# Performance work log

Measured on AMD Instinct MI355X. Metric: run time of the kernel, lower is better.

Reference implementation:

```python
import jax, jax.numpy as jnp
import numpy as np

B = 16384       # batch of weight blocks
IN = 64         # input_size == e_dim
DENC = 512      # dim_encoder
NRES = 2        # n_resblock (weights shared, see ResidualStack [block]*n)
NE = 2048       # n_embeddings
P = 12          # basis vectors per block
BETA = 0.25
SCALE = 1.0
SHIFT = 0.0


def setup_inputs() -> dict:
    key = jax.random.key(0)
    ks = jax.random.split(key, 6)
    s = 0.02
    return {
        "x": jax.random.normal(ks[0], (B, IN), dtype=jnp.float32),
        "enc_w1": jax.random.normal(ks[1], (IN, DENC), dtype=jnp.float32) * s,
        "enc_b1": jnp.zeros((DENC,), jnp.float32),
        "res_w": jax.random.normal(ks[2], (DENC, DENC), dtype=jnp.float32) * s,
        "res_b": jnp.zeros((DENC,), jnp.float32),
        "res_g": jnp.ones((DENC,), jnp.float32),
        "res_beta": jnp.zeros((DENC,), jnp.float32),
        "enc_w2": jax.random.normal(ks[3], (DENC, IN * P), dtype=jnp.float32) * s,
        "enc_b2": jnp.zeros((IN * P,), jnp.float32),
        "emb": jax.random.uniform(ks[4], (NE, IN), jnp.float32, -1.0 / NE, 1.0 / NE),
    }


def _layer_norm(r, g, b):
    mu = jnp.mean(r, axis=-1, keepdims=True)
    var = jnp.mean((r - mu) ** 2, axis=-1, keepdims=True)
    return (r - mu) * jax.lax.rsqrt(var + 1e-5) * g + b


def reference(x, enc_w1, enc_b1, res_w, res_b, res_g, res_beta, enc_w2, enc_b2, emb):
    sg = jax.lax.stop_gradient
    x_shift = (x - SHIFT) / SCALE

    # encoder: Linear -> (shared ResBlock) x NRES -> Linear
    h = x_shift @ enc_w1 + enc_b1                      # (B, DENC)
    for _ in range(NRES):
        h = h + jax.nn.relu(_layer_norm(h @ res_w + res_b, res_g, res_beta))
    z = h @ enc_w2 + enc_b2                            # (B, P*IN)

    z_e = z.reshape(B, P, IN)
    zf = z_e.reshape(-1, IN)                           # (B*P, IN)

    # pairwise squared distances to codebook, argmin, gather
    d = (jnp.sum(zf ** 2, axis=1, keepdims=True)
         + jnp.sum(emb ** 2, axis=1)
         - 2.0 * zf @ emb.T)                           # (B*P, NE)
    idx = jnp.argmin(d, axis=1)                        # (B*P,)
    z_q = emb[idx].reshape(B, P, IN)

    loss = (jnp.mean((sg(z_q) - z_e) ** 2)
            + BETA * jnp.mean((z_q - sg(z_e)) ** 2))

    # straight-through estimator
    z_q = z_e + sg(z_q - z_e)

    counts = jnp.zeros((NE,), jnp.float32).at[idx].add(1.0) / idx.shape[0]
    perplexity = jnp.exp(-jnp.sum(counts * jnp.log(counts + 1e-10)))

    # pinv-based reconstruction: A (B, IN, P), coeff = pinv(A) @ x_shift
    A = jnp.transpose(z_q, (0, 2, 1))                  # (B, IN, P)
    coeff = jnp.matmul(jnp.linalg.pinv(A), x_shift[..., None])  # (B, P, 1)
    x_hat = jnp.matmul(A, coeff)[..., 0]               # (B, IN)
    x_hat = SCALE * x_hat + SHIFT

    return (loss, x_hat, perplexity, idx, coeff)
```

## Files before the change

### kernel.cpp

```cpp
#include <hip/hip_runtime.h>
#include <math.h>

#define B_    16384
#define IN_   64
#define DENC_ 512
#define NE_   2048
#define P_    12
#define ROWS_ 196608
#define BETA_ 0.25

#define XHAT_OFF 1
#define PERP_OFF 1048577
#define IDXF_OFF 1048578
#define COEF_OFF 1245186

typedef __bf16 bf16x8 __attribute__((ext_vector_type(8)));
typedef float  f32x16 __attribute__((ext_vector_type(16)));

__device__ __forceinline__ void split3(float v, __bf16& h, __bf16& m, __bf16& l) {
    h = (__bf16)v;
    float r1 = v - (float)h;
    m = (__bf16)r1;
    float r2 = r1 - (float)m;
    l = (__bf16)r2;
}

__device__ __forceinline__ void gload_lds16(const void* g, void* l) {
    __builtin_amdgcn_global_load_lds((const __attribute__((address_space(1))) void*)g,
                                     (__attribute__((address_space(3))) void*)l, 16, 0, 0);
}

__global__ void k_wsplit(const float* __restrict__ W,
                         __bf16* __restrict__ Wh, __bf16* __restrict__ Wm,
                         __bf16* __restrict__ Wl, int kshift, int N, int total) {
    int idx = blockIdx.x * 256 + threadIdx.x;
    if (idx < total) {
        int n = idx >> kshift;
        int k = idx & ((1 << kshift) - 1);
        float v = W[(size_t)k * N + n];
        __bf16 h, m, l;
        split3(v, h, m, l);
        Wh[idx] = h; Wm[idx] = m; Wl[idx] = l;
    }
}

__global__ __launch_bounds__(256) void k_gemm_mfma(const float* __restrict__ A,
                                                   const __bf16* __restrict__ Bh,
                                                   const __bf16* __restrict__ Bm,
                                                   const __bf16* __restrict__ Bl,
                                                   const float* __restrict__ bias,
                                                   float* __restrict__ C,
                                                   int N, int K) {
    __shared__ __bf16 eS[2][3][64 * 64];

    const int tid = threadIdx.x;
    const int w = tid >> 6, lane = tid & 63;
    const int r0 = blockIdx.y * 128 + w * 32;
    const int n0 = blockIdx.x * 64;
    const int lrow = lane & 31;
    const int half = lane >> 5;

    const int cc0 = tid >> 3, qq = tid & 7;
    const int cc1 = cc0 + 32;
    const size_t off0 = (size_t)cc0 * K + (size_t)((qq ^ (cc0 & 7)) * 8);
    const size_t off1 = (size_t)cc1 * K + (size_t)((qq ^ (cc1 & 7)) * 8);
    const size_t nbase = (size_t)n0 * K;
    const int ld0 = w * 512;
    const int ld1 = 2048 + w * 512;

    f32x16 acc0, acc1;
#pragma unroll
    for (int i = 0; i < 16; ++i) { acc0[i] = 0.0f; acc1[i] = 0.0f; }

    {
        const size_t b = nbase;
        gload_lds16(Bh + b + off0, &eS[0][0][ld0]);
        gload_lds16(Bh + b + off1, &eS[0][0][ld1]);
        gload_lds16(Bm + b + off0, &eS[0][1][ld0]);
        gload_lds16(Bm + b + off1, &eS[0][1][ld1]);
        gload_lds16(Bl + b + off0, &eS[0][2][ld0]);
        gload_lds16(Bl + b + off1, &eS[0][2][ld1]);
    }

    const int nch = K >> 6;
    for (int ch = 0; ch < nch; ++ch) {
        const int cur = ch & 1;
        __syncthreads();

        if (ch + 1 < nch) {
            const int nxt = cur ^ 1;
            const size_t b = nbase + (size_t)(ch + 1) * 64;
            gload_lds16(Bh + b + off0, &eS[nxt][0][ld0]);
            gload_lds16(Bh + b + off1, &eS[nxt][0][ld1]);
            gload_lds16(Bm + b + off0, &eS[nxt][1][ld0]);
            gload_lds16(Bm + b + off1, &eS[nxt][1][ld1]);
            gload_lds16(Bl + b + off0, &eS[nxt][2][ld0]);
            gload_lds16(Bl + b + off1, &eS[nxt][2][ld1]);
        }

        bf16x8 ah[4], am[4], al[4];
        {
            const float* ar = A + (size_t)(r0 + lrow) * K + ch * 64 + half * 8;
#pragma unroll
            for (int kc = 0; kc < 4; ++kc) {
                float4 u0 = *(const float4*)(ar + kc * 16);
                float4 u1 = *(const float4*)(ar + kc * 16 + 4);
                float v[8] = {u0.x, u0.y, u0.z, u0.w, u1.x, u1.y, u1.z, u1.w};
#pragma unroll
                for (int j = 0; j < 8; ++j) {
                    __bf16 hh, mm, ll;
                    split3(v[j], hh, mm, ll);
                    ah[kc][j] = hh; am[kc][j] = mm; al[kc][j] = ll;
                }
            }
        }

#pragma unroll
        for (int kc = 0; kc < 4; ++kc) {
            const int q = kc * 2 + half;
            const int g = (q ^ (lrow & 7)) * 8;
            bf16x8 b0h = *(const bf16x8*)(&eS[cur][0][lrow * 64 + g]);
            bf16x8 b0m = *(const bf16x8*)(&eS[cur][1][lrow * 64 + g]);
            bf16x8 b0l = *(const bf16x8*)(&eS[cur][2][lrow * 64 + g]);
            bf16x8 b1h = *(const bf16x8*)(&eS[cur][0][(lrow + 32) * 64 + g]);
            bf16x8 b1m = *(const bf16x8*)(&eS[cur][1][(lrow + 32) * 64 + g]);
            bf16x8 b1l = *(const bf16x8*)(&eS[cur][2][(lrow + 32) * 64 + g]);

            acc0 = __builtin_amdgcn_mfma_f32_32x32x16_bf16(ah[kc], b0h, acc0, 0, 0, 0);
            acc1 = __builtin_amdgcn_mfma_f32_32x32x16_bf16(ah[kc], b1h, acc1, 0, 0, 0);
            acc0 = __builtin_amdgcn_mfma_f32_32x32x16_bf16(ah[kc], b0m, acc0, 0, 0, 0);
            acc1 = __builtin_amdgcn_mfma_f32_32x32x16_bf16(ah[kc], b1m, acc1, 0, 0, 0);
            acc0 = __builtin_amdgcn_mfma_f32_32x32x16_bf16(am[kc], b0h, acc0, 0, 0, 0);
            acc1 = __builtin_amdgcn_mfma_f32_32x32x16_bf16(am[kc], b1h, acc1, 0, 0, 0);
            acc0 = __builtin_amdgcn_mfma_f32_32x32x16_bf16(ah[kc], b0l, acc0, 0, 0, 0);
            acc1 = __builtin_amdgcn_mfma_f32_32x32x16_bf16(ah[kc], b1l, acc1, 0, 0, 0);
            acc0 = __builtin_amdgcn_mfma_f32_32x32x16_bf16(am[kc], b0m, acc0, 0, 0, 0);
            acc1 = __builtin_amdgcn_mfma_f32_32x32x16_bf16(am[kc], b1m, acc1, 0, 0, 0);
            acc0 = __builtin_amdgcn_mfma_f32_32x32x16_bf16(al[kc], b0h, acc0, 0, 0, 0);
            acc1 = __builtin_amdgcn_mfma_f32_32x32x16_bf16(al[kc], b1h, acc1, 0, 0, 0);
        }
    }

    const int col0 = n0 + lrow, col1 = col0 + 32;
    const float bv0 = bias[col0], bv1 = bias[col1];
#pragma unroll
    for (int r = 0; r < 16; ++r) {
        int row = r0 + (r & 3) + 8 * (r >> 2) + 4 * half;
        C[(size_t)row * N + col0] = acc0[r] + bv0;
        C[(size_t)row * N + col1] = acc1[r] + bv1;
    }
}

__global__ __launch_bounds__(256) void k_lnrelu(const float* __restrict__ t,
                                                float* __restrict__ h,
                                                const float* __restrict__ g,
                                                const float* __restrict__ beta) {
    const int tid = threadIdx.x;
    const int wv = tid >> 6, lane = tid & 63;
    const int row = blockIdx.x * 4 + wv;
    const float* tr = t + (size_t)row * DENC_;
    float* hr = h + (size_t)row * DENC_;

    float4 v0 = *(const float4*)(tr + lane * 4);
    float4 v1 = *(const float4*)(tr + 256 + lane * 4);

    float s = v0.x + v0.y + v0.z + v0.w + v1.x + v1.y + v1.z + v1.w;
#pragma unroll
    for (int m = 1; m < 64; m <<= 1) s += __shfl_xor(s, m);
    float mu = s / 512.0f;

    float d0x = v0.x - mu, d0y = v0.y - mu, d0z = v0.z - mu, d0w = v0.w - mu;
    float d1x = v1.x - mu, d1y = v1.y - mu, d1z = v1.z - mu, d1w = v1.w - mu;
    float vs = d0x * d0x + d0y * d0y + d0z * d0z + d0w * d0w +
               d1x * d1x + d1y * d1y + d1z * d1z + d1w * d1w;
#pragma unroll
    for (int m = 1; m < 64; m <<= 1) vs += __shfl_xor(vs, m);
    float var = vs / 512.0f;
    float rs = (float)(1.0 / sqrt((double)var + 1e-5));

    float4 g0 = *(const float4*)(g + lane * 4);
    float4 g1 = *(const float4*)(g + 256 + lane * 4);
    float4 b0 = *(const float4*)(beta + lane * 4);
    float4 b1 = *(const float4*)(beta + 256 + lane * 4);

    float4 h0 = *(float4*)(hr + lane * 4);
    float4 h1 = *(float4*)(hr + 256 + lane * 4);

    h0.x += fmaxf(d0x * rs * g0.x + b0.x, 0.0f);
    h0.y += fmaxf(d0y * rs * g0.y + b0.y, 0.0f);
    h0.z += fmaxf(d0z * rs * g0.z + b0.z, 0.0f);
    h0.w += fmaxf(d0w * rs * g0.w + b0.w, 0.0f);
    h1.x += fmaxf(d1x * rs * g1.x + b1.x, 0.0f);
    h1.y += fmaxf(d1y * rs * g1.y + b1.y, 0.0f);
    h1.z += fmaxf(d1z * rs * g1.z + b1.z, 0.0f);
    h1.w += fmaxf(d1w * rs * g1.w + b1.w, 0.0f);

    *(float4*)(hr + lane * 4) = h0;
    *(float4*)(hr + 256 + lane * 4) = h1;
}

__global__ __launch_bounds__(256) void k_esplit_fast(const float* __restrict__ emb,
                                                     __bf16* __restrict__ Ehi,
                                                     __bf16* __restrict__ Emid,
                                                     __bf16* __restrict__ Elo) {
    const int wv = threadIdx.x >> 6, lane = threadIdx.x & 63;
    const int c = blockIdx.x * 4 + wv;
    float v = emb[(size_t)c * 64 + lane];
    __bf16 h, m, l;
    split3(v, h, m, l);
    Ehi[(size_t)c * 64 + lane] = h;
    Emid[(size_t)c * 64 + lane] = m;
    Elo[(size_t)c * 64 + lane] = l;
}

__global__ void k_esq(const float* __restrict__ emb, float* __restrict__ se) {
    int t = blockIdx.x * 256 + threadIdx.x;
    if (t < NE_) {
        float s = 0.0f;
        for (int k = 0; k < 64; ++k) {
            float v = emb[(size_t)t * 64 + k];
            s += v * v;
        }
        se[t] = s;
    }
}

__global__ __launch_bounds__(256) void k_rowsq(const float* __restrict__ z,
                                               float* __restrict__ sz) {
    const int tid = threadIdx.x;
    const int row = blockIdx.x * 64 + (tid >> 2);
    const int part = tid & 3;
    const float4* zp = (const float4*)(z + (size_t)row * 64) + part * 4;
    float s = 0.0f;
#pragma unroll
    for (int i = 0; i < 4; ++i) {
        float4 v = zp[i];
        s += v.x * v.x + v.y * v.y + v.z * v.z + v.w * v.w;
    }
    s += __shfl_xor(s, 1);
    s += __shfl_xor(s, 2);
    if (part == 0) sz[row] = s;
}

__global__ __launch_bounds__(256) void k_distm(const float* __restrict__ z,
                                               const float* __restrict__ se,
                                               const float* __restrict__ sz,
                                               const __bf16* __restrict__ Ehi,
                                               const __bf16* __restrict__ Emid,
                                               const __bf16* __restrict__ Elo,
                                               int* __restrict__ idxw,
                                               float* __restrict__ idxf,
                                               float* __restrict__ lossacc,
                                               int* __restrict__ counts) {
    __shared__ __bf16 eS[2][3][64 * 64];

    const int tid = threadIdx.x;
    const int w = tid >> 6, lane = tid & 63;
    const int r0 = blockIdx.x * 128 + w * 32;
    const int lrow = lane & 31;
    const int half = lane >> 5;

    const int cc0 = tid >> 3, qq = tid & 7;
    const int cc1 = cc0 + 32;
    const int off0 = cc0 * 64 + (qq ^ (cc0 & 7)) * 8;
    const int off1 = cc1 * 64 + (qq ^ (cc1 & 7)) * 8;
    const int ld0 = w * 512;
    const int ld1 = 2048 + w * 512;

    bf16x8 ah[4], am[4], al[4];
    {
        const float* zr = z + (size_t)(r0 + lrow) * 64 + half * 8;
#pragma unroll
        for (int kc = 0; kc < 4; ++kc) {
            float4 u0 = *(const float4*)(zr + kc * 16);
            float4 u1 = *(const float4*)(zr + kc * 16 + 4);
            float v[8] = {u0.x, u0.y, u0.z, u0.w, u1.x, u1.y, u1.z, u1.w};
#pragma unroll
            for (int j = 0; j < 8; ++j) {
                __bf16 hh, mm, ll;
                split3(v[j], hh, mm, ll);
                ah[kc][j] = hh; am[kc][j] = mm; al[kc][j] = ll;
            }
        }
    }

    float szv[16];
#pragma unroll
    for (int r = 0; r < 16; ++r) {
        int rl = (r & 3) + 8 * (r >> 2) + 4 * half;
        szv[r] = sz[r0 + rl];
    }

    float bd[16];
    int bi[16];
#pragma unroll
    for (int r = 0; r < 16; ++r) { bd[r] = 1e30f; bi[r] = 0; }

    gload_lds16(Ehi + off0, &eS[0][0][ld0]);
    gload_lds16(Ehi + off1, &eS[0][0][ld1]);
    gload_lds16(Emid + off0, &eS[0][1][ld0]);
    gload_lds16(Emid + off1, &eS[0][1][ld1]);
    gload_lds16(Elo + off0, &eS[0][2][ld0]);
    gload_lds16(Elo + off1, &eS[0][2][ld1]);

    for (int ch = 0; ch < 32; ++ch) {
        const int cur = ch & 1;
        __syncthreads();

        if (ch + 1 < 32) {
            const int nxt = cur ^ 1;
            const int b = (ch + 1) * 4096;
            gload_lds16(Ehi + b + off0, &eS[nxt][0][ld0]);
            gload_lds16(Ehi + b + off1, &eS[nxt][0][ld1]);
            gload_lds16(Emid + b + off0, &eS[nxt][1][ld0]);
            gload_lds16(Emid + b + off1, &eS[nxt][1][ld1]);
            gload_lds16(Elo + b + off0, &eS[nxt][2][ld0]);
            gload_lds16(Elo + b + off1, &eS[nxt][2][ld1]);
        }

        f32x16 acc0, acc1;
#pragma unroll
        for (int i = 0; i < 16; ++i) { acc0[i] = 0.0f; acc1[i] = 0.0f; }

#pragma unroll
        for (int kc = 0; kc < 4; ++kc) {
            const int q = kc * 2 + half;
            const int g = (q ^ (lrow & 7)) * 8;
            bf16x8 b0h = *(const bf16x8*)(&eS[cur][0][lrow * 64 + g]);
            bf16x8 b0m = *(const bf16x8*)(&eS[cur][1][lrow * 64 + g]);
            bf16x8 b0l = *(const bf16x8*)(&eS[cur][2][lrow * 64 + g]);
            bf16x8 b1h = *(const bf16x8*)(&eS[cur][0][(lrow + 32) * 64 + g]);
            bf16x8 b1m = *(const bf16x8*)(&eS[cur][1][(lrow + 32) * 64 + g]);
            bf16x8 b1l = *(const bf16x8*)(&eS[cur][2][(lrow + 32) * 64 + g]);

            acc0 = __builtin_amdgcn_mfma_f32_32x32x16_bf16(ah[kc], b0h, acc0, 0, 0, 0);
            acc1 = __builtin_amdgcn_mfma_f32_32x32x16_bf16(ah[kc], b1h, acc1, 0, 0, 0);
            acc0 = __builtin_amdgcn_mfma_f32_32x32x16_bf16(ah[kc], b0m, acc0, 0, 0, 0);
            acc1 = __builtin_amdgcn_mfma_f32_32x32x16_bf16(ah[kc], b1m, acc1, 0, 0, 0);
            acc0 = __builtin_amdgcn_mfma_f32_32x32x16_bf16(am[kc], b0h, acc0, 0, 0, 0);
            acc1 = __builtin_amdgcn_mfma_f32_32x32x16_bf16(am[kc], b1h, acc1, 0, 0, 0);
            acc0 = __builtin_amdgcn_mfma_f32_32x32x16_bf16(ah[kc], b0l, acc0, 0, 0, 0);
            acc1 = __builtin_amdgcn_mfma_f32_32x32x16_bf16(ah[kc], b1l, acc1, 0, 0, 0);
            acc0 = __builtin_amdgcn_mfma_f32_32x32x16_bf16(am[kc], b0m, acc0, 0, 0, 0);
            acc1 = __builtin_amdgcn_mfma_f32_32x32x16_bf16(am[kc], b1m, acc1, 0, 0, 0);
            acc0 = __builtin_amdgcn_mfma_f32_32x32x16_bf16(al[kc], b0h, acc0, 0, 0, 0);
            acc1 = __builtin_amdgcn_mfma_f32_32x32x16_bf16(al[kc], b1h, acc1, 0, 0, 0);
        }

        const int c0 = ch * 64;
        const float se0 = se[c0 + lrow];
        const float se1 = se[c0 + lrow + 32];
        const int   ci0 = c0 + lrow, ci1 = c0 + lrow + 32;
#pragma unroll
        for (int r = 0; r < 16; ++r) {
            float d0 = fmaf(-2.0f, acc0[r], szv[r] + se0);
            if (d0 < bd[r]) { bd[r] = d0; bi[r] = ci0; }
            float d1 = fmaf(-2.0f, acc1[r], szv[r] + se1);
            if (d1 < bd[r]) { bd[r] = d1; bi[r] = ci1; }
        }
    }

#pragma unroll
    for (int r = 0; r < 16; ++r) {
        float d = bd[r];
        int i = bi[r];
#pragma unroll
        for (int off = 1; off < 32; off <<= 1) {
            float od = __shfl_xor(d, off);
            int oi = __shfl_xor(i, off);
            if (od < d || (od == d && oi < i)) { d = od; i = oi; }
        }
        bd[r] = d; bi[r] = i;
    }

    if (lrow == 0) {
        float lsum = 0.0f;
#pragma unroll
        for (int r = 0; r < 16; ++r) {
            int rl = (r & 3) + 8 * (r >> 2) + 4 * half;
            int row = r0 + rl;
            idxw[row] = bi[r];
            idxf[row] = (float)bi[r];
            lsum += bd[r];
            atomicAdd(&counts[bi[r]], 1);
        }
        atomicAdd(lossacc, lsum);
    }
}

__global__ __launch_bounds__(256) void k_lossperp(const float* __restrict__ lossacc,
                                                  const int* __restrict__ counts,
                                                  float* __restrict__ out) {
    __shared__ double red[256];
    const int tid = threadIdx.x;

    double hsum = 0.0;
    for (int i = tid; i < NE_; i += 256) {
        float p = (float)counts[i] / 196608.0f;
        float lg = logf(p + 1e-10f);
        hsum += (double)(p * lg);
    }
    red[tid] = hsum;
    __syncthreads();
    for (int off = 128; off > 0; off >>= 1) {
        if (tid < off) red[tid] += red[tid + off];
        __syncthreads();
    }
    if (tid == 0) {
        out[PERP_OFF] = (float)exp(-red[0]);
        out[0] = (float)((double)lossacc[0] * (1.0 + BETA_) / ((double)ROWS_ * IN_));
    }
}

__global__ __launch_bounds__(256) void k_pinv(const float* __restrict__ xin,
                                              const float* __restrict__ emb,
                                              const int* __restrict__ idxw,
                                              float* __restrict__ coeff,
                                              float* __restrict__ xhat) {
    __shared__ float aS[4][12][65];
    __shared__ float xS[4][64];
    __shared__ double GS[4][12][12];
    __shared__ double bS[4][12];
    __shared__ double uS[4][12];
    __shared__ float cS[4][12];

    const int tid = threadIdx.x;
    const int wv = tid >> 6, lane = tid & 63;
    const int b = blockIdx.x * 4 + wv;

    int my = 0;
    if (lane < 12) my = idxw[(size_t)b * 12 + lane];
    int id[12];
#pragma unroll
    for (int p = 0; p < 12; ++p) id[p] = __shfl(my, p);

    int rep = lane, mcnt = 1;
    if (lane < 12) {
        rep = -1;
        mcnt = 0;
        for (int q = 0; q < 12; ++q) {
            if (id[q] == id[lane]) {
                if (rep < 0) rep = q;
                mcnt++;
            }
        }
    }

#pragma unroll
    for (int p = 0; p < 12; ++p) aS[wv][p][lane] = emb[(size_t)id[p] * 64 + lane];
    xS[wv][lane] = xin[(size_t)b * 64 + lane];
    __syncthreads();

    for (int item = lane; item < 90; item += 64) {
        if (item < 78) {
            int j = 0, k = 0, c = item;
            for (j = 0; j < 12; ++j) {
                int cnt = 12 - j;
                if (c < cnt) { k = j + c; break; }
                c -= cnt;
            }
            double s = 0.0;
            for (int t = 0; t < 64; ++t) s += (double)aS[wv][j][t] * (double)aS[wv][k][t];
            GS[wv][j][k] = s;
            GS[wv][k][j] = s;
        } else {
            int j = item - 78;
            double s = 0.0;
            for (int t = 0; t < 64; ++t) s += (double)aS[wv][j][t] * (double)xS[wv][t];
            bS[wv][j] = s;
        }
    }
    __syncthreads();

    if (lane == 0) {
        for (int p = 0; p < 12; ++p) {
            int rp = -1;
            for (int q = 0; q < 12; ++q) {
                if (id[q] == id[p]) { rp = q; break; }
            }
            if (rp != p) {
                for (int q = 0; q < 12; ++q) {
                    GS[wv][p][q] = 0.0;
                    GS[wv][q][p] = 0.0;
                }
                GS[wv][p][p] = 1.0;
                bS[wv][p] = 0.0;
            }
        }
    }
    __syncthreads();

    for (int j = 0; j < 12; ++j) {
        if (lane == j) {
            double s = GS[wv][j][j];
            for (int k = 0; k < j; ++k) {
                double l = GS[wv][j][k];
                s -= l * l;
            }
            GS[wv][j][j] = sqrt(fmax(s, 1e-30));
        }
        __syncthreads();
        if (lane > j && lane < 12) {
            double s = GS[wv][lane][j];
            for (int k = 0; k < j; ++k) s -= GS[wv][lane][k] * GS[wv][j][k];
            GS[wv][lane][j] = s / GS[wv][j][j];
        }
        __syncthreads();
    }

    if (lane == 0) {
        double y[12];
        for (int i = 0; i < 12; ++i) {
            double s = bS[wv][i];
            for (int k = 0; k < i; ++k) s -= GS[wv][i][k] * y[k];
            y[i] = s / GS[wv][i][i];
        }
        for (int i = 11; i >= 0; --i) {
            double s = y[i];
            for (int k = i + 1; k < 12; ++k) s -= GS[wv][k][i] * uS[wv][k];
            uS[wv][i] = s / GS[wv][i][i];
        }
    }
    __syncthreads();

    if (lane < 12) {
        double c = uS[wv][rep] / (double)mcnt;
        coeff[(size_t)b * 12 + lane] = (float)c;
        cS[wv][lane] = (float)c;
    }
    __syncthreads();

    float s = 0.0f;
#pragma unroll
    for (int p = 0; p < 12; ++p) s += aS[wv][p][lane] * cS[wv][p];
    xhat[(size_t)b * 64 + lane] = s;
}


extern "C" void kernel_launch(void* const* d_in, const int* in_sizes, int n_in,
                              void* d_out, int out_size, void* d_ws, size_t ws_size,
                              hipStream_t stream) {
    const float* x        = (const float*)d_in[0];
    const float* enc_w1   = (const float*)d_in[1];
    const float* enc_b1   = (const float*)d_in[2];
    const float* res_w    = (const float*)d_in[3];
    const float* res_b    = (const float*)d_in[4];
    const float* res_g    = (const float*)d_in[5];
    const float* res_beta = (const float*)d_in[6];
    const float* enc_w2   = (const float*)d_in[7];
    const float* enc_b2   = (const float*)d_in[8];
    const float* emb      = (const float*)d_in[9];

    float* out = (float*)d_out;

    float* h  = (float*)d_ws;
    float* tz = h + (size_t)B_ * DENC_;
    float* se    = h;
    float* sz    = h + 2048;
    int*   idxw  = (int*)(h + 2048 + (size_t)ROWS_);
    int*   cnts  = (int*)(h + 2048 + 2 * (size_t)ROWS_);
    float* lossacc = (float*)(cnts + NE_);
    __bf16* Ehi  = (__bf16*)(h + 2048 + 2 * (size_t)ROWS_ + 2048 + 16);
    __bf16* Emid = Ehi + (size_t)NE_ * 64;
    __bf16* Elo  = Emid + (size_t)NE_ * 64;
    __bf16* W1h = (__bf16*)(tz + (size_t)B_ * 768);
    __bf16* W1m = W1h + (size_t)DENC_ * IN_;
    __bf16* W1l = W1m + (size_t)DENC_ * IN_;
    __bf16* Wrh = W1l + (size_t)DENC_ * IN_;
    __bf16* Wrm = Wrh + (size_t)DENC_ * DENC_;
    __bf16* Wrl = Wrm + (size_t)DENC_ * DENC_;
    __bf16* W2h = Wrl + (size_t)DENC_ * DENC_;
    __bf16* W2m = W2h + (size_t)768 * DENC_;
    __bf16* W2l = W2m + (size_t)768 * DENC_;

    float* t = tz;
    float* z = tz;

    k_wsplit<<<(DENC_ * IN_ + 255) / 256, 256, 0, stream>>>(enc_w1, W1h, W1m, W1l, 6, DENC_, DENC_ * IN_);
    k_wsplit<<<(DENC_ * DENC_ + 255) / 256, 256, 0, stream>>>(res_w, Wrh, Wrm, Wrl, 9, DENC_, DENC_ * DENC_);
    k_wsplit<<<(768 * DENC_ + 255) / 256, 256, 0, stream>>>(enc_w2, W2h, W2m, W2l, 9, 768, 768 * DENC_);

    k_gemm_mfma<<<dim3(DENC_ / 64, B_ / 128), 256, 0, stream>>>(x, W1h, W1m, W1l, enc_b1, h, DENC_, IN_);
    for (int r = 0; r < 2; ++r) {
        k_gemm_mfma<<<dim3(DENC_ / 64, B_ / 128), 256, 0, stream>>>(h, Wrh, Wrm, Wrl, res_b, t, DENC_, DENC_);
        k_lnrelu<<<B_ / 4, 256, 0, stream>>>(t, h, res_g, res_beta);
    }
    k_gemm_mfma<<<dim3(768 / 64, B_ / 128), 256, 0, stream>>>(h, W2h, W2m, W2l, enc_b2, z, 768, DENC_);

    hipMemsetAsync(cnts, 0, (NE_ + 16) * sizeof(int), stream);
    k_esplit_fast<<<NE_ / 4, 256, 0, stream>>>(emb, Ehi, Emid, Elo);
    k_esq<<<NE_ / 256, 256, 0, stream>>>(emb, se);
    k_rowsq<<<ROWS_ / 64, 256, 0, stream>>>(z, sz);
    k_distm<<<ROWS_ / 128, 256, 0, stream>>>(z, se, sz, Ehi, Emid, Elo,
                                             idxw, out + IDXF_OFF, lossacc, cnts);
    k_lossperp<<<1, 256, 0, stream>>>(lossacc, cnts, out);
    k_pinv<<<B_ / 4, 256, 0, stream>>>(x, emb, idxw, out + COEF_OFF, out + XHAT_OFF);
}
```

Baseline: 763.4 us.

## Retile distance kernel so each wave covers 64 rows by 32 codes

Changes the wave-level tiling of the distance/argmin kernel. Each wave now handles two 32-row groups against one 32-code half of each 64-code chunk, where before it handled one 32-row group against both halves. B fragments are now read from LDS once and reused across the two row groups, which halves LDS reads per MFMA. The cost is twice the A-fragment registers and a new cross-wave argmin merge through shared memory with an extra barrier.

```diff
diff --git a/kernel.cpp b/kernel.cpp
--- a/kernel.cpp
+++ b/kernel.cpp
@@ -253,10 +253,13 @@
                                                float* __restrict__ lossacc,
                                                int* __restrict__ counts) {
     __shared__ __bf16 eS[2][3][64 * 64];
+    __shared__ float mD[4][64];
+    __shared__ int   mI[4][64];
 
     const int tid = threadIdx.x;
     const int w = tid >> 6, lane = tid & 63;
-    const int r0 = blockIdx.x * 128 + w * 32;
+    const int rbase = blockIdx.x * 128 + (w >> 1) * 64;
+    const int chalf = w & 1;
     const int lrow = lane & 31;
     const int half = lane >> 5;
 
@@ -267,9 +270,10 @@
     const int ld0 = w * 512;
     const int ld1 = 2048 + w * 512;
 
-    bf16x8 ah[4], am[4], al[4];
-    {
-        const float* zr = z + (size_t)(r0 + lrow) * 64 + half * 8;
+    bf16x8 ah[2][4], am[2][4], al[2][4];
+#pragma unroll
+    for (int rg = 0; rg < 2; ++rg) {
+        const float* zr = z + (size_t)(rbase + rg * 32 + lrow) * 64 + half * 8;
 #pragma unroll
         for (int kc = 0; kc < 4; ++kc) {
             float4 u0 = *(const float4*)(zr + kc * 16);
@@ -279,22 +283,26 @@
             for (int j = 0; j < 8; ++j) {
                 __bf16 hh, mm, ll;
                 split3(v[j], hh, mm, ll);
-                ah[kc][j] = hh; am[kc][j] = mm; al[kc][j] = ll;
-            }
-        }
-    }
-
-    float szv[16];
-#pragma unroll
-    for (int r = 0; r < 16; ++r) {
-        int rl = (r & 3) + 8 * (r >> 2) + 4 * half;
-        szv[r] = sz[r0 + rl];
-    }
-
-    float bd[16];
-    int bi[16];
-#pragma unroll
-    for (int r = 0; r < 16; ++r) { bd[r] = 1e30f; bi[r] = 0; }
+                ah[rg][kc][j] = hh; am[rg][kc][j] = mm; al[rg][kc][j] = ll;
+            }
+        }
+    }
+
+    float szv[2][16];
+#pragma unroll
+    for (int rg = 0; rg < 2; ++rg)
+#pragma unroll
+        for (int r = 0; r < 16; ++r) {
+            int rl = (r & 3) + 8 * (r >> 2) + 4 * half;
+            szv[rg][r] = sz[rbase + rg * 32 + rl];
+        }
+
+    float bd[2][16];
+    int bi[2][16];
+#pragma unroll
+    for (int rg = 0; rg < 2; ++rg)
+#pragma unroll
+        for (int r = 0; r < 16; ++r) { bd[rg][r] = 1e30f; bi[rg][r] = 0; }
 
     gload_lds16(Ehi + off0, &eS[0][0][ld0]);
     gload_lds16(Ehi + off1, &eS[0][0][ld1]);
@@ -302,6 +310,8 @@
     gload_lds16(Emid + off1, &eS[0][1][ld1]);
     gload_lds16(Elo + off0, &eS[0][2][ld0]);
     gload_lds16(Elo + off1, &eS[0][2][ld1]);
+
+    const int cL = chalf * 32 + lrow;
 
     for (int ch = 0; ch < 32; ++ch) {
         const int cur = ch & 1;
@@ -325,66 +335,77 @@
 #pragma unroll
         for (int kc = 0; kc < 4; ++kc) {
             const int q = kc * 2 + half;
-            const int g = (q ^ (lrow & 7)) * 8;
-            bf16x8 b0h = *(const bf16x8*)(&eS[cur][0][lrow * 64 + g]);
-            bf16x8 b0m = *(const bf16x8*)(&eS[cur][1][lrow * 64 + g]);
-            bf16x8 b0l = *(const bf16x8*)(&eS[cur][2][lrow * 64 + g]);
-            bf16x8 b1h = *(const bf16x8*)(&eS[cur][0][(lrow + 32) * 64 + g]);
-            bf16x8 b1m = *(const bf16x8*)(&eS[cur][1][(lrow + 32) * 64 + g]);
-            bf16x8 b1l = *(const bf16x8*)(&eS[cur][2][(lrow + 32) * 64 + g]);
-
-            acc0 = __builtin_amdgcn_mfma_f32_32x32x16_bf16(ah[kc], b0h, acc0, 0, 0, 0);
-            acc1 = __builtin_amdgcn_mfma_f32_32x32x16_bf16(ah[kc], b1h, acc1, 0, 0, 0);
-            acc0 = __builtin_amdgcn_mfma_f32_32x32x16_bf16(ah[kc], b0m, acc0, 0, 0, 0);
-            acc1 = __builtin_amdgcn_mfma_f32_32x32x16_bf16(ah[kc], b1m, acc1, 0, 0, 0);
-            acc0 = __builtin_amdgcn_mfma_f32_32x32x16_bf16(am[kc], b0h, acc0, 0, 0, 0);
-            acc1 = __builtin_amdgcn_mfma_f32_32x32x16_bf16(am[kc], b1h, acc1, 0, 0, 0);
-            acc0 = __builtin_amdgcn_mfma_f32_32x32x16_bf16(ah[kc], b0l, acc0, 0, 0, 0);
-            acc1 = __builtin_amdgcn_mfma_f32_32x32x16_bf16(ah[kc], b1l, acc1, 0, 0, 0);
-            acc0 = __builtin_amdgcn_mfma_f32_32x32x16_bf16(am[kc], b0m, acc0, 0, 0, 0);
-            acc1 = __builtin_amdgcn_mfma_f32_32x32x16_bf16(am[kc], b1m, acc1, 0, 0, 0);
-            acc0 = __builtin_amdgcn_mfma_f32_32x32x16_bf16(al[kc], b0h, acc0, 0, 0, 0);
-            acc1 = __builtin_amdgcn_mfma_f32_32x32x16_bf16(al[kc], b1h, acc1, 0, 0, 0);
-        }
-
-        const int c0 = ch * 64;
-        const float se0 = se[c0 + lrow];
-        const float se1 = se[c0 + lrow + 32];
-        const int   ci0 = c0 + lrow, ci1 = c0 + lrow + 32;
+            const int base = cL * 64 + (q ^ (cL & 7)) * 8;
+            bf16x8 bh = *(const bf16x8*)(&eS[cur][0][base]);
+            bf16x8 bm = *(const bf16x8*)(&eS[cur][1][base]);
+            bf16x8 bl = *(const bf16x8*)(&eS[cur][2][base]);
+
+            acc0 = __builtin_amdgcn_mfma_f32_32x32x16_bf16(ah[0][kc], bh, acc0, 0, 0, 0);
+            acc1 = __builtin_amdgcn_mfma_f32_32x32x16_bf16(ah[1][kc], bh, acc1, 0, 0, 0);
+            acc0 = __builtin_amdgcn_mfma_f32_32x32x16_bf16(ah[0][kc], bm, acc0, 0, 0, 0);
+            acc1 = __builtin_amdgcn_mfma_f32_32x32x16_bf16(ah[1][kc], bm, acc1, 0, 0, 0);
+            acc0 = __builtin_amdgcn_mfma_f32_32x32x16_bf16(am[0][kc], bh, acc0, 0, 0, 0);
+            acc1 = __builtin_amdgcn_mfma_f32_32x32x16_bf16(am[1][kc], bh, acc1, 0, 0, 0);
+            acc0 = __builtin_amdgcn_mfma_f32_32x32x16_bf16(ah[0][kc], bl, acc0, 0, 0, 0);
+            acc1 = __builtin_amdgcn_mfma_f32_32x32x16_bf16(ah[1][kc], bl, acc1, 0, 0, 0);
+            acc0 = __builtin_amdgcn_mfma_f32_32x32x16_bf16(am[0][kc], bm, acc0, 0, 0, 0);
+            acc1 = __builtin_amdgcn_mfma_f32_32x32x16_bf16(am[1][kc], bm, acc1, 0, 0, 0);
+            acc0 = __builtin_amdgcn_mfma_f32_32x32x16_bf16(al[0][kc], bh, acc0, 0, 0, 0);
+            acc1 = __builtin_amdgcn_mfma_f32_32x32x16_bf16(al[1][kc], bh, acc1, 0, 0, 0);
+        }
+
+        const int c = ch * 64 + cL;
+        const float sec = se[c];
 #pragma unroll
         for (int r = 0; r < 16; ++r) {
-            float d0 = fmaf(-2.0f, acc0[r], szv[r] + se0);
-            if (d0 < bd[r]) { bd[r] = d0; bi[r] = ci0; }
-            float d1 = fmaf(-2.0f, acc1[r], szv[r] + se1);
-            if (d1 < bd[r]) { bd[r] = d1; bi[r] = ci1; }
-        }
-    }
-
-#pragma unroll
-    for (int r = 0; r < 16; ++r) {
-        float d = bd[r];
-        int i = bi[r];
-#pragma unroll
-        for (int off = 1; off < 32; off <<= 1) {
-            float od = __shfl_xor(d, off);
-            int oi = __shfl_xor(i, off);
-            if (od < d || (od == d && oi < i)) { d = od; i = oi; }
-        }
-        bd[r] = d; bi[r] = i;
-    }
+            float d0 = fmaf(-2.0f, acc0[r], szv[0][r] + sec);
+            if (d0 < bd[0][r]) { bd[0][r] = d0; bi[0][r] = c; }
+            float d1 = fmaf(-2.0f, acc1[r], szv[1][r] + sec);
+            if (d1 < bd[1][r]) { bd[1][r] = d1; bi[1][r] = c; }
+        }
+    }
+
+#pragma unroll
+    for (int rg = 0; rg < 2; ++rg)
+#pragma unroll
+        for (int r = 0; r < 16; ++r) {
+            float d = bd[rg][r];
+            int i = bi[rg][r];
+#pragma unroll
+            for (int off = 1; off < 32; off <<= 1) {
+                float od = __shfl_xor(d, off);
+                int oi = __shfl_xor(i, off);
+                if (od < d || (od == d && oi < i)) { d = od; i = oi; }
+            }
+            bd[rg][r] = d; bi[rg][r] = i;
+        }
 
     if (lrow == 0) {
-        float lsum = 0.0f;
-#pragma unroll
-        for (int r = 0; r < 16; ++r) {
-            int rl = (r & 3) + 8 * (r >> 2) + 4 * half;
-            int row = r0 + rl;
-            idxw[row] = bi[r];
-            idxf[row] = (float)bi[r];
-            lsum += bd[r];
-            atomicAdd(&counts[bi[r]], 1);
-        }
-        atomicAdd(lossacc, lsum);
+#pragma unroll
+        for (int rg = 0; rg < 2; ++rg)
+#pragma unroll
+            for (int r = 0; r < 16; ++r) {
+                int rl = rg * 32 + (r & 3) + 8 * (r >> 2) + 4 * half;
+                mD[w][rl] = bd[rg][r];
+                mI[w][rl] = bi[rg][r];
+            }
+    }
+    __syncthreads();
+
+    if (chalf == 0) {
+        float d0 = mD[w][lane], d1 = mD[w + 1][lane];
+        int   i0 = mI[w][lane], i1 = mI[w + 1][lane];
+        bool take1 = (d1 < d0) || (d1 == d0 && i1 < i0);
+        float d = take1 ? d1 : d0;
+        int   i = take1 ? i1 : i0;
+        int row = rbase + lane;
+        idxw[row] = i;
+        idxf[row] = (float)i;
+        atomicAdd(&counts[i], 1);
+        float s = d;
+#pragma unroll
+        for (int off = 1; off < 64; off <<= 1) s += __shfl_xor(s, off);
+        if (lane == 0) atomicAdd(lossacc, s);
     }
 }
 
```

Measured after the change: 903.0 us. 1.18x slower.
